# Kernel optimization log

Hardware: AMD Instinct MI355X
Metric: run time of the kernel (lower is better)

## Reference

```python
import jax, jax.numpy as jnp
import numpy as np

B, S, HID = 1, 2048, 4096
NH, NKV, HD = 32, 8, 128
GROUPS = NH // NKV
EPS = 1e-8
THETA = 10000.0
SCALE = HD ** -0.5
INIT = 0.02


def setup_inputs() -> dict:
    key = jax.random.key(0)
    ks = jax.random.split(key, 8)
    return {
        "hidden_states": jax.random.normal(ks[0], (B, S, HID), jnp.float32),
        "position_ids": jnp.arange(S, dtype=jnp.int32)[None, :],
        "wq": jax.random.normal(ks[1], (HID, NH * HD), jnp.float32) * INIT,
        "wk": jax.random.normal(ks[2], (HID, NKV * HD), jnp.float32) * INIT,
        "wv": jax.random.normal(ks[3], (HID, NKV * HD), jnp.float32) * INIT,
        "wo": jax.random.normal(ks[4], (NH * HD, HID), jnp.float32) * INIT,
        "memory": jax.random.normal(ks[5], (NKV, HD, HD), jnp.float32) * INIT,
        "norm_m": jax.random.uniform(ks[6], (NKV, HD, HD), jnp.float32) * 0.5 + 0.5,
        "beta": jnp.zeros((1,), jnp.float32),
    }


def _rotate_half(x):
    h = x.shape[-1] // 2
    return jnp.concatenate([-x[..., h:], x[..., :h]], axis=-1)


def _rope(position_ids):
    inv_freq = 1.0 / (THETA ** (jnp.arange(0, HD, 2, dtype=jnp.float32) / HD))  # [HD/2]
    freqs = position_ids.astype(jnp.float32)[:, :, None] * inv_freq[None, None, :]  # [B,S,HD/2]
    emb = jnp.concatenate([freqs, freqs], axis=-1)  # [B,S,HD]
    return jnp.cos(emb)[:, None], jnp.sin(emb)[:, None]  # [B,1,S,HD] each


def reference(hidden_states, position_ids, wq, wk, wv, wo, memory, norm_m, beta):
    # projections -> [B, heads, S, HD]
    q = (hidden_states @ wq).reshape(B, S, NH, HD).transpose(0, 2, 1, 3)
    k = (hidden_states @ wk).reshape(B, S, NKV, HD).transpose(0, 2, 1, 3)
    v = (hidden_states @ wv).reshape(B, S, NKV, HD).transpose(0, 2, 1, 3)

    # ---- retrieve from compressive memory (pre-RoPE Q, as in original) ----
    qf = jax.nn.elu(q) + 1.0
    qn = qf / (qf.sum(axis=-1, keepdims=True) + EPS)            # [B,NH,S,HD]
    mem_t = jnp.tile(memory[None], (1, GROUPS, 1, 1))            # torch .repeat == tile: head h -> memory[h % NKV]
    norm_t = jnp.tile(jnp.swapaxes(norm_m, -1, -2)[None], (1, GROUPS, 1, 1))
    mem_out = jnp.matmul(qn, mem_t) / (jnp.matmul(qn, norm_t) + EPS)  # [B,NH,S,HD]

    # ---- delta-rule memory update (no-grad side effect in torch) ----
    kf = jax.nn.elu(k) + 1.0
    kn = kf / (kf.sum(axis=-1, keepdims=True) + EPS)             # [B,NKV,S,HD]
    v_ret = jnp.matmul(kn, memory) / (jnp.matmul(kn, jnp.swapaxes(norm_m, -1, -2)) + EPS)
    delta = jnp.einsum('bhsd,bhse->hde', kn, v - v_ret)          # sum over batch
    updated_memory = memory + delta
    updated_norm = norm_m + kn.sum(axis=2, keepdims=True)[0]     # [NKV,1,HD] broadcast

    # ---- RoPE ----
    cos, sin = _rope(position_ids)
    q = q * cos + _rotate_half(q) * sin
    k = k * cos + _rotate_half(k) * sin

    # ---- causal attention with GQA (repeat_interleave for K/V) ----
    kr = jnp.repeat(k, GROUPS, axis=1)
    vr = jnp.repeat(v, GROUPS, axis=1)
    scores = jnp.einsum('bhqd,bhkd->bhqk', q, kr) * SCALE        # [B,NH,S,S]
    causal = jnp.tril(jnp.ones((S, S), dtype=bool))
    scores = jnp.where(causal, scores, jnp.finfo(scores.dtype).min)
    attn = jax.nn.softmax(scores, axis=-1)
    attn_out = jnp.einsum('bhqk,bhkd->bhqd', attn, vr)           # [B,NH,S,HD]

    # ---- sigmoid-gated combine + output projection ----
    gate = jax.nn.sigmoid(beta)                                   # [1]
    combined = gate * mem_out + (1.0 - gate) * attn_out
    out = combined.transpose(0, 2, 1, 3).reshape(B, S, NH * HD) @ wo
    return out, updated_memory, updated_norm
```

## Files before the change

kernel.cpp:

```cpp
#include <hip/hip_runtime.h>

#define S_LEN 2048
#define HID_DIM 4096
#define NH 32
#define NKV 8
#define HD 128
#define QKV_N 6144
#define SCALE_F 0.08838834764831845f

typedef unsigned short u16;
typedef __attribute__((ext_vector_type(8))) __bf16 bf16x8;
typedef __attribute__((ext_vector_type(4))) float f32x4;

__device__ __forceinline__ u16 f2bf(float f) {
  unsigned u = __float_as_uint(f);
  return (u16)((u + 0x7fffu + ((u >> 16) & 1u)) >> 16);
}
__device__ __forceinline__ float bf2f(u16 v) {
  return __uint_as_float((unsigned)v << 16);
}

__device__ __forceinline__ void gl_lds16(const u16* g, u16* l) {
  __builtin_amdgcn_global_load_lds(
      (const __attribute__((address_space(1))) unsigned int*)g,
      (__attribute__((address_space(3))) unsigned int*)l, 16, 0, 0);
}


__global__ void k_f32_to_bf16(const float* __restrict__ in, u16* __restrict__ out, long n4) {
  long i = (long)blockIdx.x * blockDim.x + threadIdx.x;
  if (i >= n4) return;
  float4 v = ((const float4*)in)[i];
  ushort4 o;
  o.x = f2bf(v.x); o.y = f2bf(v.y); o.z = f2bf(v.z); o.w = f2bf(v.w);
  ((ushort4*)out)[i] = o;
}

__device__ __forceinline__ void tr64_body(const float* __restrict__ A, u16* __restrict__ O,
                                          int ld_in, int ld_out, int r0, int c0, int tid) {
  __shared__ float tile[64][65];
  int tx = tid & 31, ty = tid >> 5;
#pragma unroll
  for (int i = 0; i < 8; i++) {
    int r = ty + 8 * i;
    float2 v = *(const float2*)&A[(long)(r0 + r) * ld_in + c0 + 2 * tx];
    tile[r][2 * tx] = v.x;
    tile[r][2 * tx + 1] = v.y;
  }
  __syncthreads();
#pragma unroll
  for (int i = 0; i < 8; i++) {
    int c = ty + 8 * i;
    ushort2 o;
    o.x = f2bf(tile[2 * tx][c]);
    o.y = f2bf(tile[2 * tx + 1][c]);
    *(ushort2*)&O[(long)(c0 + c) * ld_out + r0 + 2 * tx] = o;
  }
}

__global__ void k_tr64(const float* __restrict__ in, u16* __restrict__ out,
                       int ld_in, int ld_out, long in_bs, long out_bs) {
  tr64_body(in + (long)blockIdx.z * in_bs, out + (long)blockIdx.z * out_bs,
            ld_in, ld_out, blockIdx.y * 64, blockIdx.x * 64, threadIdx.x);
}

__global__ void k_trw(const float* __restrict__ wq, const float* __restrict__ wk,
                      const float* __restrict__ wv, u16* __restrict__ wT6) {
  int bid = blockIdx.x;
  const float* src; int ld, bx, by; long ooff;
  if (bid < 4096) { src = wq; ld = 4096; ooff = 0; bx = bid & 63; by = bid >> 6; }
  else if (bid < 5120) { int b = bid - 4096; src = wk; ld = 1024; ooff = (long)4096 * HID_DIM; bx = b & 15; by = b >> 4; }
  else { int b = bid - 5120; src = wv; ld = 1024; ooff = (long)5120 * HID_DIM; bx = b & 15; by = b >> 4; }
  tr64_body(src, wT6 + ooff, ld, HID_DIM, by * 64, bx * 64, threadIdx.x);
}

__global__ void k_bc(const float* __restrict__ memf, const float* __restrict__ norm,
                     u16* __restrict__ bc) {
  int bid = blockIdx.x;
  if (bid < 32) {
    int h = bid >> 2, sub = bid & 3;
    tr64_body(memf + (long)h * HD * HD, bc + (long)h * 32768,
              HD, HD, (sub >> 1) * 64, (sub & 1) * 64, threadIdx.x);
  } else {
    int cid = bid - 32;
    int h = cid >> 6, chunk = cid & 63;
    int i = chunk * 256 + threadIdx.x;
    bc[(long)h * 32768 + 16384 + i] = f2bf(norm[(long)h * 16384 + i]);
  }
}


template <int BN>
__global__ __launch_bounds__(512, 2) void k_gemm8(
    const u16* __restrict__ A, const u16* __restrict__ A2, int zsplit,
    const u16* __restrict__ Bt, void* __restrict__ Cv,
    int kloop, int lda, int ldb, int ldc,
    long strideA, long strideB, long strideC, int bmodB, int obf) {
  constexpr int NBG = BN / 64;
  constexpr int NNI = BN / 64;
  constexpr int BSTRIDE = 16384 + BN * 64;
  __shared__ __align__(16) u16 lds[2 * BSTRIDE];
  const int bz = blockIdx.z;
  const u16* Ap = (bz < zsplit) ? (A + (long)bz * strideA)
                                : (A2 + (long)(bz - zsplit) * strideA);
  const u16* Bp = Bt + (long)(bz % bmodB) * strideB;
  const long coff = (long)bz * strideC;

  const int gx = gridDim.x, gy = gridDim.y;
  const int nwg = gx * gy;
  int id = blockIdx.y * gx + blockIdx.x;
  if (!(nwg & 7)) { int q = nwg >> 3; id = (id & 7) * q + (id >> 3); }
  const int m0 = (id % gy) * 256;
  const int n0 = (id / gy) * BN;

  const int tid = threadIdx.x, wid = tid >> 6, lane = tid & 63;
  const int l15 = lane & 15, lhi = lane >> 4;
  const int wm = wid >> 2, wn = wid & 3;

  const int srow = (wid << 3) + (lane >> 3);
  const int ssw = ((lane & 7) ^ (lane >> 3)) * 8;
  auto stA = [&](int d, int g, long kt) {
    gl_lds16(Ap + (long)(m0 + g * 64 + srow) * lda + kt + ssw,
             &lds[d * BSTRIDE + (g * 64 + (wid << 3)) * 64]);
  };
  auto stB = [&](int d, int g, long kt) {
    gl_lds16(Bp + (long)(n0 + g * 64 + srow) * ldb + kt + ssw,
             &lds[d * BSTRIDE + 16384 + (g * 64 + (wid << 3)) * 64]);
  };

  const int swb = l15 & 7;
  const int aBase = (wm * 128 + l15) * 64;
  const int bBase = 16384 + (wn * (BN / 4) + l15) * 64;
  const int ko0 = (lhi ^ swb) * 8;
  const int ko1 = ((4 + lhi) ^ swb) * 8;

  const int KT = kloop >> 6;
  const int NIT = KT >> 1;

  f32x4 acc[8][NNI];
#pragma unroll
  for (int i = 0; i < 8; i++)
#pragma unroll
    for (int j = 0; j < NNI; j++) acc[i][j] = (f32x4){0.f, 0.f, 0.f, 0.f};

#pragma unroll
  for (int g = 0; g < 4; g++) stA(0, g, 0);
#pragma unroll
  for (int g = 0; g < NBG; g++) stB(0, g, 0);
#pragma unroll
  for (int g = 0; g < NBG; g++) stB(1, g, 64);
  asm volatile("s_waitcnt vmcnt(%0)" :: "i"(NBG) : "memory");
  __builtin_amdgcn_s_barrier();
  asm volatile("" ::: "memory");

  for (int t = 0; t < NIT; ++t) {
    const long kA = (long)(2 * t + 1) * 64;
    const long kB0 = (long)(2 * t + 2) * 64;
    const long kB1 = (long)(2 * t + 3) * 64;
    const bool st0 = (2 * t + 2) < KT;
    const bool st1 = (2 * t + 3) < KT;
    const bool last = (t + 1 == NIT);

    {
      const u16* lb = &lds[0];
      bf16x8 Bf[NNI][2];
#pragma unroll
      for (int p = 0; p < 4; p++) {
        if (p == 0) {
#pragma unroll
          for (int ni = 0; ni < NNI; ni++) {
            Bf[ni][0] = *(const bf16x8*)&lb[bBase + ni * 1024 + ko0];
            Bf[ni][1] = *(const bf16x8*)&lb[bBase + ni * 1024 + ko1];
          }
        }
        bf16x8 a0k0 = *(const bf16x8*)&lb[aBase + (2 * p) * 1024 + ko0];
        bf16x8 a0k1 = *(const bf16x8*)&lb[aBase + (2 * p) * 1024 + ko1];
        bf16x8 a1k0 = *(const bf16x8*)&lb[aBase + (2 * p + 1) * 1024 + ko0];
        bf16x8 a1k1 = *(const bf16x8*)&lb[aBase + (2 * p + 1) * 1024 + ko1];
        if (p == 0) { stA(1, 0, kA); stA(1, 1, kA); }
        else if (p == 1) { stA(1, 2, kA); stA(1, 3, kA); }
        else if (p == 2) { if (st0) { stB(0, 0, kB0); stB(0, 1, kB0); } }
        else {
          if (st0) { stB(0, 2, kB0); if (NBG > 3) stB(0, 3, kB0); }
        }
        asm volatile("" ::: "memory");
        if (p == 3) {
          if (last) asm volatile("s_waitcnt vmcnt(0)" ::: "memory");
          else      asm volatile("s_waitcnt vmcnt(%0)" :: "i"(NBG) : "memory");
        }
        __builtin_amdgcn_s_barrier();
        asm volatile("" ::: "memory");
        __builtin_amdgcn_s_setprio(1);
#pragma unroll
        for (int ni = 0; ni < NNI; ni++) {
          acc[2 * p][ni] = __builtin_amdgcn_mfma_f32_16x16x32_bf16(a0k0, Bf[ni][0], acc[2 * p][ni], 0, 0, 0);
          acc[2 * p][ni] = __builtin_amdgcn_mfma_f32_16x16x32_bf16(a0k1, Bf[ni][1], acc[2 * p][ni], 0, 0, 0);
          acc[2 * p + 1][ni] = __builtin_amdgcn_mfma_f32_16x16x32_bf16(a1k0, Bf[ni][0], acc[2 * p + 1][ni], 0, 0, 0);
          acc[2 * p + 1][ni] = __builtin_amdgcn_mfma_f32_16x16x32_bf16(a1k1, Bf[ni][1], acc[2 * p + 1][ni], 0, 0, 0);
        }
        __builtin_amdgcn_s_setprio(0);
        asm volatile("" ::: "memory");
        __builtin_amdgcn_s_barrier();
        asm volatile("" ::: "memory");
      }
    }
    {
      const u16* lb = &lds[BSTRIDE];
      bf16x8 Bf[NNI][2];
#pragma unroll
      for (int p = 0; p < 4; p++) {
        if (p == 0) {
#pragma unroll
          for (int ni = 0; ni < NNI; ni++) {
            Bf[ni][0] = *(const bf16x8*)&lb[bBase + ni * 1024 + ko0];
            Bf[ni][1] = *(const bf16x8*)&lb[bBase + ni * 1024 + ko1];
          }
        }
        bf16x8 a0k0 = *(const bf16x8*)&lb[aBase + (2 * p) * 1024 + ko0];
        bf16x8 a0k1 = *(const bf16x8*)&lb[aBase + (2 * p) * 1024 + ko1];
        bf16x8 a1k0 = *(const bf16x8*)&lb[aBase + (2 * p + 1) * 1024 + ko0];
        bf16x8 a1k1 = *(const bf16x8*)&lb[aBase + (2 * p + 1) * 1024 + ko1];
        if (p == 0) { if (st0) { stA(0, 0, kB0); stA(0, 1, kB0); } }
        else if (p == 1) { if (st0) { stA(0, 2, kB0); stA(0, 3, kB0); } }
        else if (p == 2) { if (st1) { stB(1, 0, kB1); stB(1, 1, kB1); } }
        else {
          if (st1) { stB(1, 2, kB1); if (NBG > 3) stB(1, 3, kB1); }
        }
        asm volatile("" ::: "memory");
        if (p == 3 && !last)
          asm volatile("s_waitcnt vmcnt(%0)" :: "i"(NBG) : "memory");
        __builtin_amdgcn_s_barrier();
        asm volatile("" ::: "memory");
        __builtin_amdgcn_s_setprio(1);
#pragma unroll
        for (int ni = 0; ni < NNI; ni++) {
          acc[2 * p][ni] = __builtin_amdgcn_mfma_f32_16x16x32_bf16(a0k0, Bf[ni][0], acc[2 * p][ni], 0, 0, 0);
          acc[2 * p][ni] = __builtin_amdgcn_mfma_f32_16x16x32_bf16(a0k1, Bf[ni][1], acc[2 * p][ni], 0, 0, 0);
          acc[2 * p + 1][ni] = __builtin_amdgcn_mfma_f32_16x16x32_bf16(a1k0, Bf[ni][0], acc[2 * p + 1][ni], 0, 0, 0);
          acc[2 * p + 1][ni] = __builtin_amdgcn_mfma_f32_16x16x32_bf16(a1k1, Bf[ni][1], acc[2 * p + 1][ni], 0, 0, 0);
        }
        __builtin_amdgcn_s_setprio(0);
        asm volatile("" ::: "memory");
        __builtin_amdgcn_s_barrier();
        asm volatile("" ::: "memory");
      }
    }
  }

#pragma unroll
  for (int mi = 0; mi < 8; mi++)
#pragma unroll
    for (int ni = 0; ni < NNI; ni++)
#pragma unroll
      for (int j = 0; j < 4; j++) {
        long row = m0 + wm * 128 + mi * 16 + lhi * 4 + j;
        long col = n0 + wn * (BN / 4) + ni * 16 + l15;
        if (obf)
          ((u16*)Cv)[coff + row * ldc + col] = f2bf(acc[mi][ni][j]);
        else
          ((float*)Cv)[coff + row * ldc + col] = acc[mi][ni][j];
      }
}


__global__ void k_addp(const u16* __restrict__ p0, const u16* __restrict__ p1,
                       float* __restrict__ out) {
  long i = ((long)blockIdx.x * 256 + threadIdx.x) * 8;
  ushort4 a0 = *(const ushort4*)&p0[i], a1 = *(const ushort4*)&p0[i + 4];
  ushort4 b0 = *(const ushort4*)&p1[i], b1 = *(const ushort4*)&p1[i + 4];
  float4 o0, o1;
  o0.x = bf2f(a0.x) + bf2f(b0.x); o0.y = bf2f(a0.y) + bf2f(b0.y);
  o0.z = bf2f(a0.z) + bf2f(b0.z); o0.w = bf2f(a0.w) + bf2f(b0.w);
  o1.x = bf2f(a1.x) + bf2f(b1.x); o1.y = bf2f(a1.y) + bf2f(b1.y);
  o1.z = bf2f(a1.z) + bf2f(b1.z); o1.w = bf2f(a1.w) + bf2f(b1.w);
  *(float4*)&out[i] = o0;
  *(float4*)&out[i + 4] = o1;
}


__global__ void k_qnrope(const float* __restrict__ qkv, const int* __restrict__ pos,
                         u16* __restrict__ qnb, u16* __restrict__ qrb,
                         u16* __restrict__ knb, u16* __restrict__ krb) {
  int s = blockIdx.x, y = blockIdx.y, l = threadIdx.x;
  bool isq = y < NH;
  int h = isq ? y : y - NH;
  const float* row = qkv + (long)s * QKV_N + (isq ? h * HD : HID_DIM + h * HD);
  float x0 = row[l], x1 = row[l + 64];
  float f0 = x0 > 0.f ? x0 + 1.f : __expf(x0);
  float f1 = x1 > 0.f ? x1 + 1.f : __expf(x1);
  float sum = f0 + f1;
#pragma unroll
  for (int m = 32; m >= 1; m >>= 1) sum += __shfl_xor(sum, m);
  float inv = 1.f / (sum + 1e-8f);
  float y0 = f0 * inv, y1 = f1 * inv;
  long o = ((long)h * S_LEN + s) * HD;
  float p = (float)pos[s];
  float ang = p * expf(-(float)l * (9.210340371976184f / 64.0f));
  float c = cosf(ang), sn = sinf(ang);
  u16 r0 = f2bf(x0 * c - x1 * sn), r1 = f2bf(x1 * c + x0 * sn);
  if (isq) {
    qnb[o + l] = f2bf(y0); qnb[o + l + 64] = f2bf(y1);
    qrb[o + l] = r0; qrb[o + l + 64] = r1;
  } else {
    knb[o + l] = f2bf(y0); knb[o + l + 64] = f2bf(y1);
    krb[o + l] = r0; krb[o + l + 64] = r1;
  }
}


__global__ __launch_bounds__(256, 2) void k_flash4(
    const u16* __restrict__ qr, const u16* __restrict__ kr,
    const u16* __restrict__ vt, const u16* __restrict__ rawq,
    const float* __restrict__ beta, u16* __restrict__ comb) {
  __shared__ u16 KV[2][16384];
  __shared__ u16 Ps[4][16 * 64];
  const int bx = blockIdx.x, h = blockIdx.y;
  const int hk = h >> 2;
  const int tid = threadIdx.x, wid = tid >> 6, lane = tid & 63;
  const int l15 = lane & 15, lhi = lane >> 4;
  const u16* qbase = qr + (long)h * S_LEN * HD;
  const u16* kb0 = kr + (long)hk * S_LEN * HD;
  const u16* vb0 = vt + (long)hk * HD * S_LEN;
  u16* P = Ps[wid];
  const float g = 1.f / (1.f + __expf(-beta[0]));

  int kr_r[4], kr_sc[4], vr_r[4], vr_sc[4];
#pragma unroll
  for (int it = 0; it < 4; it++) {
    int chunk = it * 4 + wid;
    kr_r[it] = chunk * 4 + (lane >> 4);
    kr_sc[it] = ((lane & 15) * 8) ^ ((kr_r[it] & 7) * 8);
    vr_r[it] = chunk * 8 + (lane >> 3);
    vr_sc[it] = ((lane & 7) * 8) ^ ((vr_r[it] & 7) * 8);
  }

  for (int si = 0; si < 2; si++) {
    const int s = si ? (31 - bx) : bx;
    const int qs = s * 64 + wid * 16;
    bf16x8 aq[4];
#pragma unroll
    for (int kc = 0; kc < 4; kc++)
      aq[kc] = *(const bf16x8*)&qbase[(long)(qs + l15) * HD + kc * 32 + lhi * 8];
    f32x4 accO[8];
#pragma unroll
    for (int i = 0; i < 8; i++) accO[i] = (f32x4){0.f, 0.f, 0.f, 0.f};
    float rs[4] = {0.f, 0.f, 0.f, 0.f};

    if (si) __syncthreads();
    {
      u16* Kb = KV[0];
#pragma unroll
      for (int it = 0; it < 4; it++)
        gl_lds16(kb0 + (long)kr_r[it] * HD + kr_sc[it], &Kb[(it * 4 + wid) * 512]);
#pragma unroll
      for (int it = 0; it < 4; it++)
        gl_lds16(vb0 + (long)vr_r[it] * S_LEN + vr_sc[it], &Kb[8192 + (it * 4 + wid) * 512]);
    }
    int cur = 0;

    for (int t = 0; t <= s; t++) {
      asm volatile("s_waitcnt vmcnt(0)" ::: "memory");
      __syncthreads();
      if (t < s) {
        u16* Kb = KV[cur ^ 1];
        const long kt = (long)(t + 1) * 64;
#pragma unroll
        for (int it = 0; it < 4; it++)
          gl_lds16(kb0 + (kt + kr_r[it]) * HD + kr_sc[it], &Kb[(it * 4 + wid) * 512]);
#pragma unroll
        for (int it = 0; it < 4; it++)
          gl_lds16(vb0 + (long)vr_r[it] * S_LEN + kt + vr_sc[it], &Kb[8192 + (it * 4 + wid) * 512]);
      }
      const u16* Ks = KV[cur];
      const u16* Vs = Ks + 8192;

      f32x4 accS[4];
#pragma unroll
      for (int i = 0; i < 4; i++) accS[i] = (f32x4){0.f, 0.f, 0.f, 0.f};
#pragma unroll
      for (int ni = 0; ni < 4; ni++) {
        int row = ni * 16 + l15;
#pragma unroll
        for (int kc = 0; kc < 4; kc++) {
          bf16x8 bk = *(const bf16x8*)&Ks[row * 128 + ((kc * 32 + lhi * 8) ^ ((row & 7) * 8))];
          accS[ni] = __builtin_amdgcn_mfma_f32_16x16x32_bf16(aq[kc], bk, accS[ni], 0, 0, 0);
        }
      }
      const bool diag = (t == s);
#pragma unroll
      for (int ni = 0; ni < 4; ni++) {
        int col = t * 64 + ni * 16 + l15;
#pragma unroll
        for (int j = 0; j < 4; j++) {
          int row = qs + lhi * 4 + j;
          float p = (!diag || col <= row) ? __expf(accS[ni][j] * SCALE_F) : 0.f;
          rs[j] += p;
          int pr = lhi * 4 + j;
          P[pr * 64 + ((ni * 16 + l15) ^ ((pr & 7) * 8))] = f2bf(p);
        }
      }
      asm volatile("s_waitcnt lgkmcnt(0)" ::: "memory");
      __builtin_amdgcn_sched_barrier(0);
      bf16x8 ap[2];
#pragma unroll
      for (int ks = 0; ks < 2; ks++)
        ap[ks] = *(const bf16x8*)&P[l15 * 64 + ((ks * 32 + lhi * 8) ^ ((l15 & 7) * 8))];
#pragma unroll
      for (int nj = 0; nj < 8; nj++) {
        int row = nj * 16 + l15;
#pragma unroll
        for (int ks = 0; ks < 2; ks++) {
          bf16x8 bv = *(const bf16x8*)&Vs[row * 64 + ((ks * 32 + lhi * 8) ^ ((row & 7) * 8))];
          accO[nj] = __builtin_amdgcn_mfma_f32_16x16x32_bf16(ap[ks], bv, accO[nj], 0, 0, 0);
        }
      }
      cur ^= 1;
    }
#pragma unroll
    for (int j = 0; j < 4; j++) {
      float v = rs[j];
      v += __shfl_xor(v, 1);
      v += __shfl_xor(v, 2);
      v += __shfl_xor(v, 4);
      v += __shfl_xor(v, 8);
      rs[j] = 1.f / v;
    }
#pragma unroll
    for (int nj = 0; nj < 8; nj++)
#pragma unroll
      for (int j = 0; j < 4; j++) {
        int row = qs + lhi * 4 + j;
        int col = nj * 16 + l15;
        long rb = ((long)h * S_LEN + row) * 256 + col;
        float mo = bf2f(rawq[rb]) / (bf2f(rawq[rb + 128]) + 1e-8f);
        float ao = accO[nj][j] * rs[j];
        comb[(long)row * HID_DIM + h * HD + col] = f2bf(g * mo + (1.f - g) * ao);
      }
  }
}


__global__ __launch_bounds__(256) void k_delta_part(
    const u16* __restrict__ knb, const u16* __restrict__ rawk,
    const float* __restrict__ qkv,
    float* __restrict__ dpart, float* __restrict__ npart) {
  __shared__ float knc[64][128];
  __shared__ u16 Uc[64][128];
  const int h = blockIdx.x, c = blockIdx.y, t = threadIdx.x;
  const long rb = ((long)h * S_LEN + (long)c * 64) * HD;
  const long rkb = ((long)h * S_LEN + (long)c * 64) * 256;
  const float* vb = qkv + HID_DIM + NKV * HD + h * HD + (long)c * 64 * QKV_N;
  for (int i = t; i < 1024; i += 256) {
    int r = i >> 4, cb = (i & 15) * 8;
    ushort4 k0 = *(const ushort4*)&knb[rb + (long)r * HD + cb];
    ushort4 k1 = *(const ushort4*)&knb[rb + (long)r * HD + cb + 4];
    knc[r][cb + 0] = bf2f(k0.x); knc[r][cb + 1] = bf2f(k0.y);
    knc[r][cb + 2] = bf2f(k0.z); knc[r][cb + 3] = bf2f(k0.w);
    knc[r][cb + 4] = bf2f(k1.x); knc[r][cb + 5] = bf2f(k1.y);
    knc[r][cb + 6] = bf2f(k1.z); knc[r][cb + 7] = bf2f(k1.w);
    ushort4 n0 = *(const ushort4*)&rawk[rkb + (long)r * 256 + cb];
    ushort4 n1 = *(const ushort4*)&rawk[rkb + (long)r * 256 + cb + 4];
    ushort4 dn0 = *(const ushort4*)&rawk[rkb + (long)r * 256 + 128 + cb];
    ushort4 dn1 = *(const ushort4*)&rawk[rkb + (long)r * 256 + 128 + cb + 4];
    float4 v0 = *(const float4*)&vb[(long)r * QKV_N + cb];
    float4 v1 = *(const float4*)&vb[(long)r * QKV_N + cb + 4];
    ushort4 u0, u1;
    u0.x = f2bf(v0.x - bf2f(n0.x) / (bf2f(dn0.x) + 1e-8f));
    u0.y = f2bf(v0.y - bf2f(n0.y) / (bf2f(dn0.y) + 1e-8f));
    u0.z = f2bf(v0.z - bf2f(n0.z) / (bf2f(dn0.z) + 1e-8f));
    u0.w = f2bf(v0.w - bf2f(n0.w) / (bf2f(dn0.w) + 1e-8f));
    u1.x = f2bf(v1.x - bf2f(n1.x) / (bf2f(dn1.x) + 1e-8f));
    u1.y = f2bf(v1.y - bf2f(n1.y) / (bf2f(dn1.y) + 1e-8f));
    u1.z = f2bf(v1.z - bf2f(n1.z) / (bf2f(dn1.z) + 1e-8f));
    u1.w = f2bf(v1.w - bf2f(n1.w) / (bf2f(dn1.w) + 1e-8f));
    *(ushort4*)&Uc[r][cb] = u0;
    *(ushort4*)&Uc[r][cb + 4] = u1;
  }
  __syncthreads();

  const int e = t & 127, dh = (t >> 7) * 64;
  float acc[64];
#pragma unroll
  for (int d = 0; d < 64; d++) acc[d] = 0.f;
  for (int s = 0; s < 64; s++) {
    float u = bf2f(Uc[s][e]);
#pragma unroll
    for (int dq = 0; dq < 16; dq++) {
      float4 k4 = *(const float4*)&knc[s][dh + dq * 4];
      acc[dq * 4 + 0] += k4.x * u;
      acc[dq * 4 + 1] += k4.y * u;
      acc[dq * 4 + 2] += k4.z * u;
      acc[dq * 4 + 3] += k4.w * u;
    }
  }
  long ob = (((long)c * NKV + h) * 128 + dh) * 128 + e;
#pragma unroll
  for (int d = 0; d < 64; d++) dpart[ob + (long)d * 128] = acc[d];

  {
    int j = e, half = t >> 7;
    float cs = 0.f;
#pragma unroll
    for (int s = 0; s < 32; s++) cs += knc[half * 32 + s][j];
    npart[(((long)c * 2 + half) * NKV + h) * 128 + j] = cs;
  }
}

__global__ void k_finish(const float* __restrict__ dpart, const float* __restrict__ npart,
                         const float* __restrict__ mem, const float* __restrict__ norm,
                         float* __restrict__ outmem, float* __restrict__ outn) {
  int bid = blockIdx.x;
  if (bid < 512) {
    long i = (long)bid * 256 + threadIdx.x;
    const long N = (long)NKV * HD * HD;
    float a = 0.f;
#pragma unroll 8
    for (int c = 0; c < 32; c++) a += dpart[(long)c * N + i];
    outmem[i] = mem[i] + a;
  } else {
    int b2 = bid - 512;
    int h = b2 >> 6, y = b2 & 63;
    int j = threadIdx.x & 127;
    int r = y * 2 + (threadIdx.x >> 7);
    float cs = 0.f;
#pragma unroll 8
    for (int cc = 0; cc < 64; cc++) cs += npart[((long)cc * NKV + h) * 128 + j];
    long o = (long)h * HD * HD + (long)r * HD + j;
    outn[o] = norm[o] + cs;
  }
}


extern "C" void kernel_launch(void* const* d_in, const int* in_sizes, int n_in,
                              void* d_out, int out_size, void* d_ws, size_t ws_size,
                              hipStream_t stream) {
  const float* hs = (const float*)d_in[0];
  const int* pos = (const int*)d_in[1];
  const float* wq = (const float*)d_in[2];
  const float* wk = (const float*)d_in[3];
  const float* wv = (const float*)d_in[4];
  const float* wo = (const float*)d_in[5];
  const float* memf = (const float*)d_in[6];
  const float* normf = (const float*)d_in[7];
  const float* beta = (const float*)d_in[8];
  (void)in_sizes; (void)n_in; (void)out_size; (void)ws_size;

  float* out = (float*)d_out;
  float* out_mem = out + (long)S_LEN * HID_DIM;
  float* out_norm = out_mem + NKV * HD * HD;

  const size_t MB = 1u << 20;
  char* w = (char*)d_ws;
  u16* hsb    = (u16*)(w + 0);
  u16* qnb    = (u16*)(w + 0);
  u16* comb   = (u16*)(w + 0);
  u16* wT6    = (u16*)(w + 16 * MB);
  u16* rawq   = (u16*)(w + 16 * MB);
  u16* woT    = (u16*)(w + 16 * MB);
  u16* rawk   = (u16*)(w + 48 * MB);
  u16* bc     = (u16*)(w + 57 * MB);
  u16* vtb    = (u16*)(w + 57 * MB + 512 * 1024);
  float* qkvf = (float*)(w + 66 * MB + 512 * 1024);
  u16* p0     = (u16*)(w + 98 * MB + 512 * 1024);
  u16* qrb    = (u16*)(w + 130 * MB + 512 * 1024);
  float* dpart= (float*)(w + 130 * MB + 512 * 1024);
  u16* p1     = (u16*)(w + 130 * MB + 512 * 1024);
  u16* krb    = (u16*)(w + 146 * MB + 512 * 1024);
  float* npart= (float*)(w + 146 * MB + 512 * 1024);
  u16* knb    = (u16*)(w + 150 * MB + 512 * 1024);

  k_f32_to_bf16<<<dim3((S_LEN * HID_DIM / 4 + 255) / 256), dim3(256), 0, stream>>>(
      hs, hsb, (long)(S_LEN * HID_DIM / 4));
  k_trw<<<dim3(6144), dim3(256), 0, stream>>>(wq, wk, wv, wT6);
  k_gemm8<192><<<dim3(QKV_N / 192, S_LEN / 256, 1), dim3(512), 0, stream>>>(
      hsb, hsb, 1 << 30, wT6, qkvf, HID_DIM, HID_DIM, HID_DIM, QKV_N,
      0L, 0L, 0L, 1, 0);

  k_qnrope<<<dim3(S_LEN, NH + NKV), dim3(64), 0, stream>>>(
      qkvf, pos, qnb, qrb, knb, krb);

  k_tr64<<<dim3(2, 32, NKV), dim3(256), 0, stream>>>(
      qkvf + HID_DIM + NKV * HD, vtb, QKV_N, S_LEN, 128L, (long)(HD * S_LEN));
  k_bc<<<dim3(544), dim3(256), 0, stream>>>(memf, normf, bc);

  k_gemm8<256><<<dim3(1, 8, NH + NKV), dim3(512), 0, stream>>>(
      qnb, knb, NH, bc, rawq, HD, HD, HD, 256,
      (long)(S_LEN * HD), (long)(256 * HD), (long)(S_LEN * 256), NKV, 1);

  k_flash4<<<dim3(16, NH), dim3(256), 0, stream>>>(qrb, krb, vtb, rawq, beta, comb);

  k_delta_part<<<dim3(NKV, 32), dim3(256), 0, stream>>>(knb, rawk, qkvf, dpart, npart);
  k_finish<<<dim3(1024), dim3(256), 0, stream>>>(dpart, npart, memf, normf, out_mem, out_norm);

  k_tr64<<<dim3(64, 64, 1), dim3(256), 0, stream>>>(
      wo, woT, HID_DIM, HID_DIM, 0L, 0L);
  k_gemm8<256><<<dim3(HID_DIM / 256, S_LEN / 256, 2), dim3(512), 0, stream>>>(
      comb, comb, 1 << 30, woT, p0, 2048, HID_DIM, HID_DIM, HID_DIM,
      2048L, 2048L, (long)(p1 - p0), 2, 1);
  k_addp<<<dim3(S_LEN * HID_DIM / 2048), dim3(256), 0, stream>>>(p0, p1, out);
}
```

Baseline: 363.1 us.

## Store QKV projection output in bf16 and merge small prep kernels

The QKV GEMM now writes a bf16 output instead of fp32, and every downstream consumer (qnrope, the V transpose, delta_part) reads the bf16 buffer. This halves the memory traffic of the QKV intermediate. The hidden-state conversion is folded into the weight-transpose kernel, and the V transpose is folded into the memory/norm prep kernel, which removes two launches. The cost is lower precision for V, and for Q/K before normalisation and RoPE.

```diff
diff --git a/kernel.cpp b/kernel.cpp
--- a/kernel.cpp
+++ b/kernel.cpp
@@ -27,15 +27,6 @@
 }
 
 
-__global__ void k_f32_to_bf16(const float* __restrict__ in, u16* __restrict__ out, long n4) {
-  long i = (long)blockIdx.x * blockDim.x + threadIdx.x;
-  if (i >= n4) return;
-  float4 v = ((const float4*)in)[i];
-  ushort4 o;
-  o.x = f2bf(v.x); o.y = f2bf(v.y); o.z = f2bf(v.z); o.w = f2bf(v.w);
-  ((ushort4*)out)[i] = o;
-}
-
 __device__ __forceinline__ void tr64_body(const float* __restrict__ A, u16* __restrict__ O,
                                           int ld_in, int ld_out, int r0, int c0, int tid) {
   __shared__ float tile[64][65];
@@ -58,31 +49,69 @@
   }
 }
 
+__device__ __forceinline__ void tr64u_body(const u16* __restrict__ A, u16* __restrict__ O,
+                                           int ld_in, int ld_out, int r0, int c0, int tid) {
+  __shared__ u16 tileu[64][66];
+  int tx = tid & 31, ty = tid >> 5;
+#pragma unroll
+  for (int i = 0; i < 8; i++) {
+    int r = ty + 8 * i;
+    ushort2 v = *(const ushort2*)&A[(long)(r0 + r) * ld_in + c0 + 2 * tx];
+    tileu[r][2 * tx] = v.x;
+    tileu[r][2 * tx + 1] = v.y;
+  }
+  __syncthreads();
+#pragma unroll
+  for (int i = 0; i < 8; i++) {
+    int c = ty + 8 * i;
+    ushort2 o;
+    o.x = tileu[2 * tx][c];
+    o.y = tileu[2 * tx + 1][c];
+    *(ushort2*)&O[(long)(c0 + c) * ld_out + r0 + 2 * tx] = o;
+  }
+}
+
 __global__ void k_tr64(const float* __restrict__ in, u16* __restrict__ out,
                        int ld_in, int ld_out, long in_bs, long out_bs) {
   tr64_body(in + (long)blockIdx.z * in_bs, out + (long)blockIdx.z * out_bs,
             ld_in, ld_out, blockIdx.y * 64, blockIdx.x * 64, threadIdx.x);
 }
 
-__global__ void k_trw(const float* __restrict__ wq, const float* __restrict__ wk,
-                      const float* __restrict__ wv, u16* __restrict__ wT6) {
+__global__ void k_prep(const float* __restrict__ hs, u16* __restrict__ hsb,
+                       const float* __restrict__ wq, const float* __restrict__ wk,
+                       const float* __restrict__ wv, u16* __restrict__ wT6) {
   int bid = blockIdx.x;
-  const float* src; int ld, bx, by; long ooff;
-  if (bid < 4096) { src = wq; ld = 4096; ooff = 0; bx = bid & 63; by = bid >> 6; }
-  else if (bid < 5120) { int b = bid - 4096; src = wk; ld = 1024; ooff = (long)4096 * HID_DIM; bx = b & 15; by = b >> 4; }
-  else { int b = bid - 5120; src = wv; ld = 1024; ooff = (long)5120 * HID_DIM; bx = b & 15; by = b >> 4; }
-  tr64_body(src, wT6 + ooff, ld, HID_DIM, by * 64, bx * 64, threadIdx.x);
-}
-
-__global__ void k_bc(const float* __restrict__ memf, const float* __restrict__ norm,
-                     u16* __restrict__ bc) {
+  if (bid < 6144) {
+    const float* src; int ld, bx, by; long ooff;
+    if (bid < 4096) { src = wq; ld = 4096; ooff = 0; bx = bid & 63; by = bid >> 6; }
+    else if (bid < 5120) { int b = bid - 4096; src = wk; ld = 1024; ooff = (long)4096 * HID_DIM; bx = b & 15; by = b >> 4; }
+    else { int b = bid - 5120; src = wv; ld = 1024; ooff = (long)5120 * HID_DIM; bx = b & 15; by = b >> 4; }
+    tr64_body(src, wT6 + ooff, ld, HID_DIM, by * 64, bx * 64, threadIdx.x);
+  } else {
+    long i = (long)(bid - 6144) * 256 + threadIdx.x;
+    float4 v = ((const float4*)hs)[i];
+    ushort4 o;
+    o.x = f2bf(v.x); o.y = f2bf(v.y); o.z = f2bf(v.z); o.w = f2bf(v.w);
+    ((ushort4*)hsb)[i] = o;
+  }
+}
+
+__global__ void k_mid(const u16* __restrict__ qkvb, u16* __restrict__ vtb,
+                      const float* __restrict__ memf, const float* __restrict__ norm,
+                      u16* __restrict__ bc) {
   int bid = blockIdx.x;
-  if (bid < 32) {
-    int h = bid >> 2, sub = bid & 3;
+  if (bid < 512) {
+    int z = bid >> 6, sub = bid & 63;
+    int bx = sub & 1, by = sub >> 1;
+    tr64u_body(qkvb + HID_DIM + NKV * HD + z * HD, vtb + (long)z * HD * S_LEN,
+               QKV_N, S_LEN, by * 64, bx * 64, threadIdx.x);
+  } else if (bid < 544) {
+    int b = bid - 512;
+    int h = b >> 2, sub = b & 3;
     tr64_body(memf + (long)h * HD * HD, bc + (long)h * 32768,
               HD, HD, (sub >> 1) * 64, (sub & 1) * 64, threadIdx.x);
   } else {
-    int cid = bid - 32;
+    int cid = bid - 544;
     int h = cid >> 6, chunk = cid & 63;
     int i = chunk * 256 + threadIdx.x;
     bc[(long)h * 32768 + 16384 + i] = f2bf(norm[(long)h * 16384 + i]);
@@ -278,14 +307,14 @@
 }
 
 
-__global__ void k_qnrope(const float* __restrict__ qkv, const int* __restrict__ pos,
+__global__ void k_qnrope(const u16* __restrict__ qkv, const int* __restrict__ pos,
                          u16* __restrict__ qnb, u16* __restrict__ qrb,
                          u16* __restrict__ knb, u16* __restrict__ krb) {
   int s = blockIdx.x, y = blockIdx.y, l = threadIdx.x;
   bool isq = y < NH;
   int h = isq ? y : y - NH;
-  const float* row = qkv + (long)s * QKV_N + (isq ? h * HD : HID_DIM + h * HD);
-  float x0 = row[l], x1 = row[l + 64];
+  const u16* row = qkv + (long)s * QKV_N + (isq ? h * HD : HID_DIM + h * HD);
+  float x0 = bf2f(row[l]), x1 = bf2f(row[l + 64]);
   float f0 = x0 > 0.f ? x0 + 1.f : __expf(x0);
   float f1 = x1 > 0.f ? x1 + 1.f : __expf(x1);
   float sum = f0 + f1;
@@ -442,14 +471,14 @@
 
 __global__ __launch_bounds__(256) void k_delta_part(
     const u16* __restrict__ knb, const u16* __restrict__ rawk,
-    const float* __restrict__ qkv,
+    const u16* __restrict__ qkvb,
     float* __restrict__ dpart, float* __restrict__ npart) {
   __shared__ float knc[64][128];
   __shared__ u16 Uc[64][128];
   const int h = blockIdx.x, c = blockIdx.y, t = threadIdx.x;
   const long rb = ((long)h * S_LEN + (long)c * 64) * HD;
   const long rkb = ((long)h * S_LEN + (long)c * 64) * 256;
-  const float* vb = qkv + HID_DIM + NKV * HD + h * HD + (long)c * 64 * QKV_N;
+  const u16* vb = qkvb + HID_DIM + NKV * HD + h * HD + (long)c * 64 * QKV_N;
   for (int i = t; i < 1024; i += 256) {
     int r = i >> 4, cb = (i & 15) * 8;
     ushort4 k0 = *(const ushort4*)&knb[rb + (long)r * HD + cb];
@@ -462,17 +491,17 @@
     ushort4 n1 = *(const ushort4*)&rawk[rkb + (long)r * 256 + cb + 4];
     ushort4 dn0 = *(const ushort4*)&rawk[rkb + (long)r * 256 + 128 + cb];
     ushort4 dn1 = *(const ushort4*)&rawk[rkb + (long)r * 256 + 128 + cb + 4];
-    float4 v0 = *(const float4*)&vb[(long)r * QKV_N + cb];
-    float4 v1 = *(const float4*)&vb[(long)r * QKV_N + cb + 4];
+    ushort4 v0 = *(const ushort4*)&vb[(long)r * QKV_N + cb];
+    ushort4 v1 = *(const ushort4*)&vb[(long)r * QKV_N + cb + 4];
     ushort4 u0, u1;
-    u0.x = f2bf(v0.x - bf2f(n0.x) / (bf2f(dn0.x) + 1e-8f));
-    u0.y = f2bf(v0.y - bf2f(n0.y) / (bf2f(dn0.y) + 1e-8f));
-    u0.z = f2bf(v0.z - bf2f(n0.z) / (bf2f(dn0.z) + 1e-8f));
-    u0.w = f2bf(v0.w - bf2f(n0.w) / (bf2f(dn0.w) + 1e-8f));
-    u1.x = f2bf(v1.x - bf2f(n1.x) / (bf2f(dn1.x) + 1e-8f));
-    u1.y = f2bf(v1.y - bf2f(n1.y) / (bf2f(dn1.y) + 1e-8f));
-    u1.z = f2bf(v1.z - bf2f(n1.z) / (bf2f(dn1.z) + 1e-8f));
-    u1.w = f2bf(v1.w - bf2f(n1.w) / (bf2f(dn1.w) + 1e-8f));
+    u0.x = f2bf(bf2f(v0.x) - bf2f(n0.x) / (bf2f(dn0.x) + 1e-8f));
+    u0.y = f2bf(bf2f(v0.y) - bf2f(n0.y) / (bf2f(dn0.y) + 1e-8f));
+    u0.z = f2bf(bf2f(v0.z) - bf2f(n0.z) / (bf2f(dn0.z) + 1e-8f));
+    u0.w = f2bf(bf2f(v0.w) - bf2f(n0.w) / (bf2f(dn0.w) + 1e-8f));
+    u1.x = f2bf(bf2f(v1.x) - bf2f(n1.x) / (bf2f(dn1.x) + 1e-8f));
+    u1.y = f2bf(bf2f(v1.y) - bf2f(n1.y) / (bf2f(dn1.y) + 1e-8f));
+    u1.z = f2bf(bf2f(v1.z) - bf2f(n1.z) / (bf2f(dn1.z) + 1e-8f));
+    u1.w = f2bf(bf2f(v1.w) - bf2f(n1.w) / (bf2f(dn1.w) + 1e-8f));
     *(ushort4*)&Uc[r][cb] = u0;
     *(ushort4*)&Uc[r][cb + 4] = u1;
   }
@@ -560,8 +589,8 @@
   u16* rawk   = (u16*)(w + 48 * MB);
   u16* bc     = (u16*)(w + 57 * MB);
   u16* vtb    = (u16*)(w + 57 * MB + 512 * 1024);
-  float* qkvf = (float*)(w + 66 * MB + 512 * 1024);
-  u16* p0     = (u16*)(w + 98 * MB + 512 * 1024);
+  u16* qkvb   = (u16*)(w + 66 * MB + 512 * 1024);
+  u16* p0     = (u16*)(w + 90 * MB + 512 * 1024);
   u16* qrb    = (u16*)(w + 130 * MB + 512 * 1024);
   float* dpart= (float*)(w + 130 * MB + 512 * 1024);
   u16* p1     = (u16*)(w + 130 * MB + 512 * 1024);
@@ -569,19 +598,15 @@
   float* npart= (float*)(w + 146 * MB + 512 * 1024);
   u16* knb    = (u16*)(w + 150 * MB + 512 * 1024);
 
-  k_f32_to_bf16<<<dim3((S_LEN * HID_DIM / 4 + 255) / 256), dim3(256), 0, stream>>>(
-      hs, hsb, (long)(S_LEN * HID_DIM / 4));
-  k_trw<<<dim3(6144), dim3(256), 0, stream>>>(wq, wk, wv, wT6);
+  k_prep<<<dim3(14336), dim3(256), 0, stream>>>(hs, hsb, wq, wk, wv, wT6);
   k_gemm8<192><<<dim3(QKV_N / 192, S_LEN / 256, 1), dim3(512), 0, stream>>>(
-      hsb, hsb, 1 << 30, wT6, qkvf, HID_DIM, HID_DIM, HID_DIM, QKV_N,
-      0L, 0L, 0L, 1, 0);
+      hsb, hsb, 1 << 30, wT6, qkvb, HID_DIM, HID_DIM, HID_DIM, QKV_N,
+      0L, 0L, 0L, 1, 1);
 
   k_qnrope<<<dim3(S_LEN, NH + NKV), dim3(64), 0, stream>>>(
-      qkvf, pos, qnb, qrb, knb, krb);
-
-  k_tr64<<<dim3(2, 32, NKV), dim3(256), 0, stream>>>(
-      qkvf + HID_DIM + NKV * HD, vtb, QKV_N, S_LEN, 128L, (long)(HD * S_LEN));
-  k_bc<<<dim3(544), dim3(256), 0, stream>>>(memf, normf, bc);
+      qkvb, pos, qnb, qrb, knb, krb);
+
+  k_mid<<<dim3(1056), dim3(256), 0, stream>>>(qkvb, vtb, memf, normf, bc);
 
   k_gemm8<256><<<dim3(1, 8, NH + NKV), dim3(512), 0, stream>>>(
       qnb, knb, NH, bc, rawq, HD, HD, HD, 256,
@@ -589,7 +614,7 @@
 
   k_flash4<<<dim3(16, NH), dim3(256), 0, stream>>>(qrb, krb, vtb, rawq, beta, comb);
 
-  k_delta_part<<<dim3(NKV, 32), dim3(256), 0, stream>>>(knb, rawk, qkvf, dpart, npart);
+  k_delta_part<<<dim3(NKV, 32), dim3(256), 0, stream>>>(knb, rawk, qkvb, dpart, npart);
   k_finish<<<dim3(1024), dim3(256), 0, stream>>>(dpart, npart, memf, normf, out_mem, out_norm);
 
   k_tr64<<<dim3(64, 64, 1), dim3(256), 0, stream>>>(
```

Result: no change. 356.5 us (-1.8%).
